# Optimization experiments

Measured on AMD Instinct MI355X. Metric: run time of the kernel, lower is better.

The kernel has to match this reference:

```python
import jax, jax.numpy as jnp
import numpy as np

ROT_DIM = 32
THETA = 10000.0
HEAD_SIZE = 192


def _rope(t):
    # t: [B, T, D]; rotate first ROT_DIM features with interleaved-pair RoPE
    T = t.shape[1]
    inv_freq = 1.0 / (THETA ** (jnp.arange(0, ROT_DIM, 2, dtype=jnp.float32) / ROT_DIM))  # [16]
    freqs = jnp.arange(T, dtype=jnp.float32)[:, None] * inv_freq[None, :]  # [T,16]
    freqs = jnp.repeat(freqs, 2, axis=-1)  # [T,32], each freq repeated for the pair
    cos = jnp.cos(freqs).astype(t.dtype)
    sin = jnp.sin(freqs).astype(t.dtype)
    x = t[..., :ROT_DIM]
    x1 = x[..., 0::2]
    x2 = x[..., 1::2]
    rot_half = jnp.stack([-x2, x1], axis=-1).reshape(x.shape)  # interleave (-x2, x1)
    rotated = x * cos + rot_half * sin
    return jnp.concatenate([rotated, t[..., ROT_DIM:]], axis=-1)


def setup_inputs() -> dict:
    key = jax.random.key(0)
    k1, k2, k3, k4 = jax.random.split(key, 4)
    B, T, C, H = 64, 512, 768, HEAD_SIZE
    x = jax.random.normal(k1, (B, T, C), dtype=jnp.float32)
    s = 1.0 / np.sqrt(C)
    Wq = jax.random.normal(k2, (C, H), dtype=jnp.float32) * s
    Wk = jax.random.normal(k3, (C, H), dtype=jnp.float32) * s
    Wv = jax.random.normal(k4, (C, H), dtype=jnp.float32) * s
    return {"x": x, "Wq": Wq, "Wk": Wk, "Wv": Wv}


def reference(x, Wq, Wk, Wv):
    B, T, C = x.shape
    q = x @ Wq  # [B,T,H]
    k = x @ Wk
    v = x @ Wv
    q = _rope(q)
    k = _rope(k)
    scale = k.shape[-1] ** -0.5
    scores = jnp.einsum('bqh,bkh->bqk', q, k) * scale  # [B,T,T]
    causal = jnp.tril(jnp.ones((T, T), dtype=bool))
    scores = jnp.where(causal[None, :, :], scores, -jnp.inf)
    weight = jax.nn.softmax(scores, axis=-1)
    # dropout is identity at eval time
    out = jnp.einsum('bqk,bkh->bqh', weight, v)  # [B,T,H]
    return out
```

## Files before the change

kernel.cpp:

```cpp
#include <hip/hip_runtime.h>
#include <cstdint>

typedef __attribute__((ext_vector_type(8))) short short8;
typedef __attribute__((ext_vector_type(4))) float floatx4;

__device__ __forceinline__ unsigned short f2bf(float f) {
  uint32_t u = __builtin_bit_cast(uint32_t, f);
  u += 0x7fffu + ((u >> 16) & 1u);
  return (unsigned short)(u >> 16);
}
__device__ __forceinline__ uint32_t pkbf(float lo, float hi) {
  uint32_t a = __builtin_bit_cast(uint32_t, lo) + 0x8000u;
  uint32_t b = __builtin_bit_cast(uint32_t, hi) + 0x8000u;
  return __builtin_amdgcn_perm(b, a, 0x07060302);
}
__device__ __forceinline__ void gll16(const void* g, void* l) {
  __builtin_amdgcn_global_load_lds(
      (const __attribute__((address_space(1))) unsigned int*)g,
      (__attribute__((address_space(3))) unsigned int*)l, 16, 0, 0);
}

__global__ void prep_w_kernel(const float* __restrict__ Wq,
                              const float* __restrict__ Wk,
                              const float* __restrict__ Wv,
                              unsigned short* __restrict__ Wt) {
  int id = blockIdx.x * 256 + threadIdx.x;
  int by = id / 27648, rem = id - by * 27648;
  int kb = rem / 1152, s = rem - kb * 1152;
  int row = s >> 2, cs = s & 3;
  int n = by * 288 + row;
  int c = cs ^ ((row >> 1) & 3);
  int which = n / 192, nn = n - which * 192;
  const float* W = (which == 0) ? Wq : (which == 1) ? Wk : Wv;
  int k0 = kb * 32 + c * 8;
  unsigned short v[8];
#pragma unroll
  for (int e = 0; e < 8; ++e) v[e] = f2bf(W[(size_t)(k0 + e) * 192 + nn]);
  uint4 o;
  o.x = v[0] | ((uint32_t)v[1] << 16);
  o.y = v[2] | ((uint32_t)v[3] << 16);
  o.z = v[4] | ((uint32_t)v[5] << 16);
  o.w = v[6] | ((uint32_t)v[7] << 16);
  *(uint4*)(Wt + (size_t)id * 8) = o;
}

__global__ __launch_bounds__(256, 3) void proj_kernel(
    const float* __restrict__ x, const unsigned short* __restrict__ Wt,
    unsigned short* __restrict__ q_ws, unsigned short* __restrict__ k_ws,
    unsigned short* __restrict__ v_ws) {
  __shared__ __align__(16) unsigned short A_lds[2][64 * 32];
  __shared__ __align__(16) unsigned short B_lds[2][288 * 32];
  const int tid = threadIdx.x;
  const int w = tid >> 6, l = tid & 63, quad = l >> 4, ln = l & 15;
  const int wr = w & 1, wc = w >> 1;
  const int m0 = blockIdx.x * 64;

  const int arow = tid >> 2, ac = tid & 3;
  const int aslot = ((ac ^ ((arow >> 1) & 3)) << 4);
  const float* xp = x + (size_t)(m0 + arow) * 768 + ac * 8;
  const unsigned short* wimg = Wt + (size_t)blockIdx.y * 27648 * 8;

  const int fq = ((quad ^ ((ln >> 1) & 3)) << 4);

  floatx4 acc[2][9];
#pragma unroll
  for (int mi = 0; mi < 2; ++mi)
#pragma unroll
    for (int nj = 0; nj < 9; ++nj) acc[mi][nj] = floatx4{0.f, 0.f, 0.f, 0.f};

  float4 a0x, a0y;

#define LOADA(K0)                                  \
  do {                                             \
    a0x = *(const float4*)(xp + (K0));             \
    a0y = *(const float4*)(xp + (K0) + 4);         \
  } while (0)
#define STAGEA(BUF)                                               \
  do {                                                            \
    uint4 ap;                                                     \
    ap.x = pkbf(a0x.x, a0x.y);                                    \
    ap.y = pkbf(a0x.z, a0x.w);                                    \
    ap.z = pkbf(a0y.x, a0y.y);                                    \
    ap.w = pkbf(a0y.z, a0y.w);                                    \
    *(uint4*)((char*)&A_lds[BUF][0] + arow * 64 + aslot) = ap;    \
  } while (0)
#define LOADB(KB, BUF)                                               \
  do {                                                               \
    const unsigned short* src = wimg + (size_t)(KB) * 9216;          \
    char* dstb = (char*)&B_lds[BUF][0];                              \
    _Pragma("unroll") for (int it = 0; it < 4; ++it)                 \
        gll16(src + (it * 256 + tid) * 8, dstb + (it * 256 + tid) * 16); \
    if (tid < 128) gll16(src + (1024 + tid) * 8, dstb + (1024 + tid) * 16); \
  } while (0)
#define PCOMPUTE(BUF)                                                            \
  do {                                                                           \
    short8 af0 = *(const short8*)((const char*)&A_lds[BUF][0] +                  \
                                  (wr * 32 + ln) * 64 + fq);                     \
    short8 af1 = *(const short8*)((const char*)&A_lds[BUF][0] +                  \
                                  (wr * 32 + 16 + ln) * 64 + fq);                \
    _Pragma("unroll") for (int nj = 0; nj < 9; ++nj) {                           \
      short8 bf = *(const short8*)((const char*)&B_lds[BUF][0] +                 \
                                   (wc * 144 + nj * 16 + ln) * 64 + fq);         \
      acc[0][nj] = __builtin_amdgcn_mfma_f32_16x16x32_bf16(af0, bf, acc[0][nj],  \
                                                           0, 0, 0);             \
      acc[1][nj] = __builtin_amdgcn_mfma_f32_16x16x32_bf16(af1, bf, acc[1][nj],  \
                                                           0, 0, 0);             \
    }                                                                            \
  } while (0)

  LOADB(0, 0);
  LOADA(0);
  STAGEA(0);
  LOADA(32);
  __syncthreads();

#pragma unroll 2
  for (int kb = 0; kb < 24; ++kb) {
    const int cur = kb & 1, nxt = cur ^ 1;
    if (kb < 23) {
      LOADB(kb + 1, nxt);
      STAGEA(nxt);
    }
    if (kb < 22) LOADA((kb + 2) * 32);
    PCOMPUTE(cur);
    __syncthreads();
  }
#undef LOADA
#undef STAGEA
#undef LOADB
#undef PCOMPUTE

  const float R_LG = 0.8304820237218406f;
#define ROPE2(V0, V1, TPOS)                                         \
  do {                                                              \
    float i0 = (float)(ln >> 1);                                    \
    float f0 = exp2f(-i0 * R_LG);                                   \
    float f1 = exp2f(-(i0 + 8.0f) * R_LG);                          \
    float s0, c0, s1, c1;                                           \
    sincosf((float)(TPOS)*f0, &s0, &c0);                            \
    sincosf((float)(TPOS)*f1, &s1, &c1);                            \
    float p0 = __shfl_xor(V0, 1), p1 = __shfl_xor(V1, 1);           \
    V0 = (ln & 1) ? (V0 * c0 + p0 * s0) : (V0 * c0 - p0 * s0);      \
    V1 = (ln & 1) ? (V1 * c1 + p1 * s1) : (V1 * c1 - p1 * s1);      \
  } while (0)

  const int role = blockIdx.y * 2 + wc;
  if (role == 0) {
#pragma unroll
    for (int mi = 0; mi < 2; ++mi)
#pragma unroll
      for (int r = 0; r < 4; ++r) {
        int row_g = m0 + wr * 32 + mi * 16 + quad * 4 + r;
        int t_pos = row_g & 511;
        float v0 = acc[mi][0][r], v1 = acc[mi][1][r];
        ROPE2(v0, v1, t_pos);
        q_ws[(size_t)row_g * 192 + ln] = f2bf(v0);
        q_ws[(size_t)row_g * 192 + 16 + ln] = f2bf(v1);
#pragma unroll
        for (int nj = 2; nj < 9; ++nj)
          q_ws[(size_t)row_g * 192 + nj * 16 + ln] = f2bf(acc[mi][nj][r]);
      }
  } else if (role == 1) {
#pragma unroll
    for (int mi = 0; mi < 2; ++mi)
#pragma unroll
      for (int r = 0; r < 4; ++r) {
        int row_g = m0 + wr * 32 + mi * 16 + quad * 4 + r;
        int t_pos = row_g & 511;
        float v0 = acc[mi][3][r], v1 = acc[mi][4][r];
        ROPE2(v0, v1, t_pos);
#pragma unroll
        for (int nj = 0; nj < 3; ++nj)
          q_ws[(size_t)row_g * 192 + 144 + nj * 16 + ln] = f2bf(acc[mi][nj][r]);
        k_ws[(size_t)row_g * 192 + ln] = f2bf(v0);
        k_ws[(size_t)row_g * 192 + 16 + ln] = f2bf(v1);
#pragma unroll
        for (int nj = 5; nj < 9; ++nj)
          k_ws[(size_t)row_g * 192 + (nj - 3) * 16 + ln] = f2bf(acc[mi][nj][r]);
      }
  } else if (role == 2) {
#pragma unroll
    for (int mi = 0; mi < 2; ++mi) {
#pragma unroll
      for (int r = 0; r < 4; ++r) {
        int row_g = m0 + wr * 32 + mi * 16 + quad * 4 + r;
#pragma unroll
        for (int nj = 0; nj < 6; ++nj)
          k_ws[(size_t)row_g * 192 + 96 + nj * 16 + ln] = f2bf(acc[mi][nj][r]);
      }
      int rb = m0 + wr * 32 + mi * 16 + quad * 4;
      int bb = rb >> 9, t = rb & 511;
#pragma unroll
      for (int nj = 6; nj < 9; ++nj) {
        ushort4 pv;
        pv.x = f2bf(acc[mi][nj][0]);
        pv.y = f2bf(acc[mi][nj][1]);
        pv.z = f2bf(acc[mi][nj][2]);
        pv.w = f2bf(acc[mi][nj][3]);
        *(ushort4*)&v_ws[((size_t)bb * 192 + (nj - 6) * 16 + ln) * 512 + t] = pv;
      }
    }
  } else {
#pragma unroll
    for (int mi = 0; mi < 2; ++mi) {
      int rb = m0 + wr * 32 + mi * 16 + quad * 4;
      int bb = rb >> 9, t = rb & 511;
#pragma unroll
      for (int nj = 0; nj < 9; ++nj) {
        ushort4 pv;
        pv.x = f2bf(acc[mi][nj][0]);
        pv.y = f2bf(acc[mi][nj][1]);
        pv.z = f2bf(acc[mi][nj][2]);
        pv.w = f2bf(acc[mi][nj][3]);
        *(ushort4*)&v_ws[((size_t)bb * 192 + 48 + nj * 16 + ln) * 512 + t] = pv;
      }
    }
  }
#undef ROPE2
}

__global__ __launch_bounds__(256) void attn_kernel(
    const unsigned short* __restrict__ q_ws, const unsigned short* __restrict__ k_ws,
    const unsigned short* __restrict__ v_ws, float* __restrict__ out) {
  __shared__ __align__(16) unsigned short K_lds[64 * 200];
  __shared__ __align__(16) unsigned short V_lds[192 * 72];
  __shared__ __align__(16) unsigned short P_lds[4][16 * 72];
  const int tid = threadIdx.x;
  const int w = tid >> 6, l = tid & 63, quad = l >> 4, ln = l & 15;
  const int b = blockIdx.y;
  const int qt = (blockIdx.y < 32) ? blockIdx.x : 7 - blockIdx.x;
  const int q0 = qt * 64;

  short8 qf[6];
  {
    const unsigned short* qp =
        q_ws + (size_t)(b * 512 + q0 + w * 16 + ln) * 192 + quad * 8;
#pragma unroll
    for (int kk = 0; kk < 6; ++kk) qf[kk] = *(const short8*)(qp + kk * 32);
  }

  float m_i[4], l_i[4];
  floatx4 o[12];
#pragma unroll
  for (int r = 0; r < 4; ++r) { m_i[r] = -1e30f; l_i[r] = 0.f; }
#pragma unroll
  for (int nt = 0; nt < 12; ++nt) o[nt] = floatx4{0.f, 0.f, 0.f, 0.f};
  const float sm_scale = 0.07216878364870323f;

  for (int kt = 0; kt <= qt; ++kt) {
    const int k0 = kt * 64;
    __syncthreads();
#pragma unroll
    for (int it = 0; it < 6; ++it) {
      int idx = it * 256 + tid;
      int row = idx / 24, c = idx - row * 24;
      uint4 v = *(const uint4*)(k_ws + (size_t)(b * 512 + k0 + row) * 192 + c * 8);
      *(uint4*)&K_lds[row * 200 + c * 8] = v;
    }
#pragma unroll
    for (int it = 0; it < 6; ++it) {
      int idx = it * 256 + tid;
      int row = idx >> 3, c = idx & 7;
      uint4 v = *(const uint4*)(v_ws + (size_t)(b * 192 + row) * 512 + k0 + c * 8);
      *(uint4*)&V_lds[row * 72 + c * 8] = v;
    }
    __syncthreads();

    float s[4][4];
    __builtin_amdgcn_s_setprio(1);
#pragma unroll
    for (int nt = 0; nt < 4; ++nt) {
      floatx4 sa = floatx4{0.f, 0.f, 0.f, 0.f};
#pragma unroll
      for (int kk = 0; kk < 6; ++kk) {
        short8 kf = *(const short8*)&K_lds[(nt * 16 + ln) * 200 + kk * 32 + quad * 8];
        sa = __builtin_amdgcn_mfma_f32_16x16x32_bf16(qf[kk], kf, sa, 0, 0, 0);
      }
#pragma unroll
      for (int r = 0; r < 4; ++r) s[nt][r] = sa[r] * sm_scale;
    }
    __builtin_amdgcn_s_setprio(0);
    if (kt == qt) {
#pragma unroll
      for (int nt = 0; nt < 4; ++nt)
#pragma unroll
        for (int r = 0; r < 4; ++r)
          if (nt * 16 + ln > w * 16 + quad * 4 + r) s[nt][r] = -1e30f;
    }
    float alpha[4];
#pragma unroll
    for (int r = 0; r < 4; ++r) {
      float mx = fmaxf(fmaxf(s[0][r], s[1][r]), fmaxf(s[2][r], s[3][r]));
      mx = fmaxf(mx, __shfl_xor(mx, 1));
      mx = fmaxf(mx, __shfl_xor(mx, 2));
      mx = fmaxf(mx, __shfl_xor(mx, 4));
      mx = fmaxf(mx, __shfl_xor(mx, 8));
      float mnew = fmaxf(m_i[r], mx);
      alpha[r] = __expf(m_i[r] - mnew);
      float sum = 0.f;
#pragma unroll
      for (int nt = 0; nt < 4; ++nt) {
        s[nt][r] = __expf(s[nt][r] - mnew);
        sum += s[nt][r];
      }
      sum += __shfl_xor(sum, 1);
      sum += __shfl_xor(sum, 2);
      sum += __shfl_xor(sum, 4);
      sum += __shfl_xor(sum, 8);
      l_i[r] = l_i[r] * alpha[r] + sum;
      m_i[r] = mnew;
    }
#pragma unroll
    for (int nt = 0; nt < 12; ++nt)
#pragma unroll
      for (int r = 0; r < 4; ++r) o[nt][r] *= alpha[r];

#pragma unroll
    for (int nt = 0; nt < 4; ++nt)
#pragma unroll
      for (int r = 0; r < 4; ++r)
        P_lds[w][(quad * 4 + r) * 72 + nt * 16 + ln] = f2bf(s[nt][r]);
    __asm__ volatile("s_waitcnt lgkmcnt(0)" ::: "memory");

    __builtin_amdgcn_s_setprio(1);
#pragma unroll
    for (int ks = 0; ks < 2; ++ks) {
      short8 pf = *(const short8*)&P_lds[w][ln * 72 + ks * 32 + quad * 8];
#pragma unroll
      for (int nt = 0; nt < 12; ++nt) {
        short8 vf = *(const short8*)&V_lds[(nt * 16 + ln) * 72 + ks * 32 + quad * 8];
        o[nt] = __builtin_amdgcn_mfma_f32_16x16x32_bf16(pf, vf, o[nt], 0, 0, 0);
      }
    }
    __builtin_amdgcn_s_setprio(0);
  }

#pragma unroll
  for (int r = 0; r < 4; ++r) {
    float inv = 1.0f / l_i[r];
    size_t rowoff = (size_t)(b * 512 + q0 + w * 16 + quad * 4 + r) * 192;
#pragma unroll
    for (int nt = 0; nt < 12; ++nt)
      out[rowoff + nt * 16 + ln] = o[nt][r] * inv;
  }
}

extern "C" void kernel_launch(void* const* d_in, const int* in_sizes, int n_in,
                              void* d_out, int out_size, void* d_ws, size_t ws_size,
                              hipStream_t stream) {
  const float* x = (const float*)d_in[0];
  const float* Wq = (const float*)d_in[1];
  const float* Wk = (const float*)d_in[2];
  const float* Wv = (const float*)d_in[3];
  float* out = (float*)d_out;

  char* ws = (char*)d_ws;
  const size_t QKV_BYTES = (size_t)64 * 512 * 192 * 2;
  unsigned short* q_ws = (unsigned short*)(ws);
  unsigned short* k_ws = (unsigned short*)(ws + QKV_BYTES);
  unsigned short* v_ws = (unsigned short*)(ws + 2 * QKV_BYTES);
  unsigned short* Wt = (unsigned short*)(ws + 3 * QKV_BYTES);

  hipLaunchKernelGGL(prep_w_kernel, dim3(216), dim3(256), 0, stream, Wq, Wk, Wv, Wt);
  hipLaunchKernelGGL(proj_kernel, dim3(512, 2), dim3(256), 0, stream, x, Wt, q_ws, k_ws, v_ws);
  hipLaunchKernelGGL(attn_kernel, dim3(8, 64), dim3(256), 0, stream, q_ws, k_ws, v_ws, out);
}
```

Baseline: 229.4 us.

## Split QKV projection into three 192-column slices per block

```diff
diff --git a/kernel.cpp b/kernel.cpp
--- a/kernel.cpp
+++ b/kernel.cpp
@@ -25,17 +25,15 @@
                               const float* __restrict__ Wv,
                               unsigned short* __restrict__ Wt) {
   int id = blockIdx.x * 256 + threadIdx.x;
-  int by = id / 27648, rem = id - by * 27648;
-  int kb = rem / 1152, s = rem - kb * 1152;
+  int bz = id / 18432, rem = id - bz * 18432;
+  int kb = rem / 768, s = rem - kb * 768;
   int row = s >> 2, cs = s & 3;
-  int n = by * 288 + row;
   int c = cs ^ ((row >> 1) & 3);
-  int which = n / 192, nn = n - which * 192;
-  const float* W = (which == 0) ? Wq : (which == 1) ? Wk : Wv;
+  const float* W = (bz == 0) ? Wq : (bz == 1) ? Wk : Wv;
   int k0 = kb * 32 + c * 8;
   unsigned short v[8];
 #pragma unroll
-  for (int e = 0; e < 8; ++e) v[e] = f2bf(W[(size_t)(k0 + e) * 192 + nn]);
+  for (int e = 0; e < 8; ++e) v[e] = f2bf(W[(size_t)(k0 + e) * 192 + row]);
   uint4 o;
   o.x = v[0] | ((uint32_t)v[1] << 16);
   o.y = v[2] | ((uint32_t)v[3] << 16);
@@ -44,29 +42,30 @@
   *(uint4*)(Wt + (size_t)id * 8) = o;
 }
 
-__global__ __launch_bounds__(256, 3) void proj_kernel(
+__global__ __launch_bounds__(256, 5) void proj_kernel(
     const float* __restrict__ x, const unsigned short* __restrict__ Wt,
     unsigned short* __restrict__ q_ws, unsigned short* __restrict__ k_ws,
     unsigned short* __restrict__ v_ws) {
   __shared__ __align__(16) unsigned short A_lds[2][64 * 32];
-  __shared__ __align__(16) unsigned short B_lds[2][288 * 32];
+  __shared__ __align__(16) unsigned short B_lds[2][192 * 32];
   const int tid = threadIdx.x;
   const int w = tid >> 6, l = tid & 63, quad = l >> 4, ln = l & 15;
   const int wr = w & 1, wc = w >> 1;
   const int m0 = blockIdx.x * 64;
+  const int bz = blockIdx.y;
 
   const int arow = tid >> 2, ac = tid & 3;
   const int aslot = ((ac ^ ((arow >> 1) & 3)) << 4);
   const float* xp = x + (size_t)(m0 + arow) * 768 + ac * 8;
-  const unsigned short* wimg = Wt + (size_t)blockIdx.y * 27648 * 8;
+  const unsigned short* wimg = Wt + (size_t)bz * 18432 * 8;
 
   const int fq = ((quad ^ ((ln >> 1) & 3)) << 4);
 
-  floatx4 acc[2][9];
+  floatx4 acc[2][6];
 #pragma unroll
   for (int mi = 0; mi < 2; ++mi)
 #pragma unroll
-    for (int nj = 0; nj < 9; ++nj) acc[mi][nj] = floatx4{0.f, 0.f, 0.f, 0.f};
+    for (int nj = 0; nj < 6; ++nj) acc[mi][nj] = floatx4{0.f, 0.f, 0.f, 0.f};
 
   float4 a0x, a0y;
 
@@ -86,11 +85,10 @@
   } while (0)
 #define LOADB(KB, BUF)                                               \
   do {                                                               \
-    const unsigned short* src = wimg + (size_t)(KB) * 9216;          \
+    const unsigned short* src = wimg + (size_t)(KB) * 6144;          \
     char* dstb = (char*)&B_lds[BUF][0];                              \
-    _Pragma("unroll") for (int it = 0; it < 4; ++it)                 \
+    _Pragma("unroll") for (int it = 0; it < 3; ++it)                 \
         gll16(src + (it * 256 + tid) * 8, dstb + (it * 256 + tid) * 16); \
-    if (tid < 128) gll16(src + (1024 + tid) * 8, dstb + (1024 + tid) * 16); \
   } while (0)
 #define PCOMPUTE(BUF)                                                            \
   do {                                                                           \
@@ -98,9 +96,9 @@
                                   (wr * 32 + ln) * 64 + fq);                     \
     short8 af1 = *(const short8*)((const char*)&A_lds[BUF][0] +                  \
                                   (wr * 32 + 16 + ln) * 64 + fq);                \
-    _Pragma("unroll") for (int nj = 0; nj < 9; ++nj) {                           \
+    _Pragma("unroll") for (int nj = 0; nj < 6; ++nj) {                           \
       short8 bf = *(const short8*)((const char*)&B_lds[BUF][0] +                 \
-                                   (wc * 144 + nj * 16 + ln) * 64 + fq);         \
+                                   (wc * 96 + nj * 16 + ln) * 64 + fq);          \
       acc[0][nj] = __builtin_amdgcn_mfma_f32_16x16x32_bf16(af0, bf, acc[0][nj],  \
                                                            0, 0, 0);             \
       acc[1][nj] = __builtin_amdgcn_mfma_f32_16x16x32_bf16(af1, bf, acc[1][nj],  \
@@ -144,75 +142,48 @@
     V1 = (ln & 1) ? (V1 * c1 + p1 * s1) : (V1 * c1 - p1 * s1);      \
   } while (0)
 
-  const int role = blockIdx.y * 2 + wc;
-  if (role == 0) {
-#pragma unroll
-    for (int mi = 0; mi < 2; ++mi)
-#pragma unroll
-      for (int r = 0; r < 4; ++r) {
-        int row_g = m0 + wr * 32 + mi * 16 + quad * 4 + r;
-        int t_pos = row_g & 511;
-        float v0 = acc[mi][0][r], v1 = acc[mi][1][r];
-        ROPE2(v0, v1, t_pos);
-        q_ws[(size_t)row_g * 192 + ln] = f2bf(v0);
-        q_ws[(size_t)row_g * 192 + 16 + ln] = f2bf(v1);
-#pragma unroll
-        for (int nj = 2; nj < 9; ++nj)
-          q_ws[(size_t)row_g * 192 + nj * 16 + ln] = f2bf(acc[mi][nj][r]);
-      }
-  } else if (role == 1) {
-#pragma unroll
-    for (int mi = 0; mi < 2; ++mi)
-#pragma unroll
-      for (int r = 0; r < 4; ++r) {
-        int row_g = m0 + wr * 32 + mi * 16 + quad * 4 + r;
-        int t_pos = row_g & 511;
-        float v0 = acc[mi][3][r], v1 = acc[mi][4][r];
-        ROPE2(v0, v1, t_pos);
-#pragma unroll
-        for (int nj = 0; nj < 3; ++nj)
-          q_ws[(size_t)row_g * 192 + 144 + nj * 16 + ln] = f2bf(acc[mi][nj][r]);
-        k_ws[(size_t)row_g * 192 + ln] = f2bf(v0);
-        k_ws[(size_t)row_g * 192 + 16 + ln] = f2bf(v1);
-#pragma unroll
-        for (int nj = 5; nj < 9; ++nj)
-          k_ws[(size_t)row_g * 192 + (nj - 3) * 16 + ln] = f2bf(acc[mi][nj][r]);
-      }
-  } else if (role == 2) {
+  if (bz < 2) {
+    unsigned short* dst = (bz == 0) ? q_ws : k_ws;
+    if (wc == 0) {
+#pragma unroll
+      for (int mi = 0; mi < 2; ++mi)
+#pragma unroll
+        for (int r = 0; r < 4; ++r) {
+          int row_g = m0 + wr * 32 + mi * 16 + quad * 4 + r;
+          int t_pos = row_g & 511;
+          float v0 = acc[mi][0][r], v1 = acc[mi][1][r];
+          ROPE2(v0, v1, t_pos);
+          dst[(size_t)row_g * 192 + ln] = f2bf(v0);
+          dst[(size_t)row_g * 192 + 16 + ln] = f2bf(v1);
+#pragma unroll
+          for (int nj = 2; nj < 6; ++nj)
+            dst[(size_t)row_g * 192 + nj * 16 + ln] = f2bf(acc[mi][nj][r]);
+        }
+    } else {
+#pragma unroll
+      for (int mi = 0; mi < 2; ++mi)
+#pragma unroll
+        for (int r = 0; r < 4; ++r) {
+          int row_g = m0 + wr * 32 + mi * 16 + quad * 4 + r;
+#pragma unroll
+          for (int nj = 0; nj < 6; ++nj)
+            dst[(size_t)row_g * 192 + 96 + nj * 16 + ln] = f2bf(acc[mi][nj][r]);
+        }
+    }
+  } else {
+    const int dbase = wc * 96;
 #pragma unroll
     for (int mi = 0; mi < 2; ++mi) {
-#pragma unroll
-      for (int r = 0; r < 4; ++r) {
-        int row_g = m0 + wr * 32 + mi * 16 + quad * 4 + r;
-#pragma unroll
-        for (int nj = 0; nj < 6; ++nj)
-          k_ws[(size_t)row_g * 192 + 96 + nj * 16 + ln] = f2bf(acc[mi][nj][r]);
-      }
       int rb = m0 + wr * 32 + mi * 16 + quad * 4;
       int bb = rb >> 9, t = rb & 511;
 #pragma unroll
-      for (int nj = 6; nj < 9; ++nj) {
+      for (int nj = 0; nj < 6; ++nj) {
         ushort4 pv;
         pv.x = f2bf(acc[mi][nj][0]);
         pv.y = f2bf(acc[mi][nj][1]);
         pv.z = f2bf(acc[mi][nj][2]);
         pv.w = f2bf(acc[mi][nj][3]);
-        *(ushort4*)&v_ws[((size_t)bb * 192 + (nj - 6) * 16 + ln) * 512 + t] = pv;
-      }
-    }
-  } else {
-#pragma unroll
-    for (int mi = 0; mi < 2; ++mi) {
-      int rb = m0 + wr * 32 + mi * 16 + quad * 4;
-      int bb = rb >> 9, t = rb & 511;
-#pragma unroll
-      for (int nj = 0; nj < 9; ++nj) {
-        ushort4 pv;
-        pv.x = f2bf(acc[mi][nj][0]);
-        pv.y = f2bf(acc[mi][nj][1]);
-        pv.z = f2bf(acc[mi][nj][2]);
-        pv.w = f2bf(acc[mi][nj][3]);
-        *(ushort4*)&v_ws[((size_t)bb * 192 + 48 + nj * 16 + ln) * 512 + t] = pv;
+        *(ushort4*)&v_ws[((size_t)bb * 192 + dbase + nj * 16 + ln) * 512 + t] = pv;
       }
     }
   }
@@ -362,6 +333,6 @@
   unsigned short* Wt = (unsigned short*)(ws + 3 * QKV_BYTES);
 
   hipLaunchKernelGGL(prep_w_kernel, dim3(216), dim3(256), 0, stream, Wq, Wk, Wv, Wt);
-  hipLaunchKernelGGL(proj_kernel, dim3(512, 2), dim3(256), 0, stream, x, Wt, q_ws, k_ws, v_ws);
+  hipLaunchKernelGGL(proj_kernel, dim3(512, 3), dim3(256), 0, stream, x, Wt, q_ws, k_ws, v_ws);
   hipLaunchKernelGGL(attn_kernel, dim3(8, 64), dim3(256), 0, stream, q_ws, k_ws, v_ws, out);
 }
```

Result: slower. 236.5 us (+3.1%).
